# Kernel optimization log

Hardware: AMD Instinct MI355X
Metric: run time of the kernel (lower is better)

Reference implementation:

```python
import jax, jax.numpy as jnp
import numpy as np

N = 100000      # nodes (categories_nums[0])
E = 1600000     # edges
FEAT = 16       # features_num
HID = 32        # hidden
IDE = 16        # id_embed_size
EMB = 8         # embed_size
CAT_MAX = 1000  # categorical vocab (categories_nums[1:])
K = 3           # TAGConv hops (sparse=False)
NC = 2          # num_class
IN_DIM = IDE + 2 * EMB + HID  # 64 -> TAGConv input
EPS = 1e-5


def layer_norm(x, g, b):
    m = jnp.mean(x, axis=-1, keepdims=True)
    v = jnp.mean((x - m) ** 2, axis=-1, keepdims=True)
    return (x - m) * jax.lax.rsqrt(v + EPS) * g + b


def setup_inputs() -> dict:
    key = jax.random.key(0)
    ks = jax.random.split(key, 20)
    s = 0.05
    return {
        "x": jax.random.normal(ks[0], (N, FEAT), jnp.float32),
        "edge_index": jax.random.randint(ks[1], (2, E), 0, N, jnp.int64),
        "edge_weight": jax.random.uniform(ks[2], (E,), jnp.float32),
        "categories_value": jax.random.randint(ks[3], (N, 3), 0, CAT_MAX, jnp.int64),
        "id_table": jax.random.normal(ks[4], (N, IDE), jnp.float32) * s,
        "lin0_id_W": jax.random.normal(ks[5], (IDE, IDE), jnp.float32) * s,
        "lin0_id_b": jnp.zeros((IDE,), jnp.float32),
        "emb1": jax.random.normal(ks[6], (CAT_MAX, EMB), jnp.float32) * s,
        "emb2": jax.random.normal(ks[7], (CAT_MAX, EMB), jnp.float32) * s,
        "lin0_emb_W": jax.random.normal(ks[8], (2 * EMB, 2 * EMB), jnp.float32) * s,
        "lin0_emb_b": jnp.zeros((2 * EMB,), jnp.float32),
        "lin0_W": jax.random.normal(ks[9], (FEAT, HID), jnp.float32) * s,
        "lin0_b": jnp.zeros((HID,), jnp.float32),
        "ln0_g": jnp.ones((IN_DIM,), jnp.float32),
        "ln0_b": jnp.zeros((IN_DIM,), jnp.float32),
        "tag_W": jax.random.normal(ks[10], (K + 1, IN_DIM, HID), jnp.float32) * s,
        "tag_b": jnp.zeros((HID,), jnp.float32),
        "ln1_g": jnp.ones((HID,), jnp.float32),
        "ln1_b": jnp.zeros((HID,), jnp.float32),
        "lin1_W": jax.random.normal(ks[11], (HID, NC), jnp.float32) * s,
        "lin1_b": jnp.zeros((NC,), jnp.float32),
    }


def reference(x, edge_index, edge_weight, categories_value, id_table, lin0_id_W,
              lin0_id_b, emb1, emb2, lin0_emb_W, lin0_emb_b, lin0_W, lin0_b,
              ln0_g, ln0_b, tag_W, tag_b, ln1_g, ln1_b, lin1_W, lin1_b):
    # eval mode: dropouts are identity
    h = jax.nn.elu(x @ lin0_W + lin0_b)                       # [N, HID]
    ide = id_table[categories_value[:, 0]]                    # [N, IDE]
    ide = jax.nn.elu(ide @ lin0_id_W + lin0_id_b)
    er = jnp.concatenate([emb1[categories_value[:, 1]],
                          emb2[categories_value[:, 2]]], axis=1)  # [N, 2*EMB]
    er = jax.nn.elu(er @ lin0_emb_W + lin0_emb_b)
    feat = jnp.concatenate([ide, h, er], axis=1)              # [N, IN_DIM]
    feat = layer_norm(feat, ln0_g, ln0_b)

    # TAGConv: gcn_norm without self-loops, K-hop propagation
    row, col = edge_index[0], edge_index[1]                   # source -> target
    deg = jax.ops.segment_sum(edge_weight, col, num_segments=N)
    dis = jnp.where(deg > 0, deg ** -0.5, 0.0)
    norm = dis[row] * edge_weight * dis[col]                  # [E]

    out = feat @ tag_W[0]                                     # [N, HID]
    xk = feat
    for k in range(1, K + 1):
        xk = jax.ops.segment_sum(xk[row] * norm[:, None], col, num_segments=N)
        out = out + xk @ tag_W[k]
    out = out + tag_b

    out = jax.nn.relu(out)
    out = layer_norm(out, ln1_g, ln1_b)
    out = out @ lin1_W + lin1_b                               # [N, NC]
    return jax.nn.log_softmax(out, axis=-1)
```

## Files before the change

kernel.cpp:

```cpp
#include <hip/hip_runtime.h>
#include <hip/hip_bf16.h>

typedef unsigned short u16;
typedef unsigned int   u32;
typedef unsigned long long u64;
typedef u32 u32x2 __attribute__((ext_vector_type(2)));
typedef u32 u32x4 __attribute__((ext_vector_type(4)));

#define FIX_SCALE 16777216.0f
#define FIX_INV   (1.0f / 16777216.0f)
#define CNT_SHIFT 40
#define DEG_MASK  ((1ULL << CNT_SHIFT) - 1)

__device__ __forceinline__ float b2f(u16 u) { return __uint_as_float(((u32)u) << 16); }
__device__ __forceinline__ u16 f2b(float f) {
    u32 u = __float_as_uint(f);
    return (u16)((u + 0x7FFFu + ((u >> 16) & 1u)) >> 16);
}
__device__ __forceinline__ float elu(float v) { return v > 0.f ? v : expm1f(v); }
__device__ __forceinline__ float ldf(const void* p, size_t i, int f32) {
    return f32 ? ((const float*)p)[i] : b2f(((const u16*)p)[i]);
}
__device__ __forceinline__ float plo(u32 a) { return __uint_as_float(a << 16); }
__device__ __forceinline__ float phi(u32 a) { return __uint_as_float(a & 0xFFFF0000u); }

__global__ void k_flags(const u32* __restrict__ gw, const int* __restrict__ ei,
                        const int* __restrict__ cat, int* __restrict__ flags) {
    if (threadIdx.x == 0 && blockIdx.x == 0) {
        flags[0] = (gw[0] == 0x3F800000u) ? 1 : 0;
        flags[1] = ((ei[1]  | ei[3]  | ei[5]  | ei[7])  == 0) ? 2 : 1;
        flags[2] = ((cat[1] | cat[3] | cat[5] | cat[7]) == 0) ? 2 : 1;
    }
}

__global__ __launch_bounds__(256) void k_feathist(
    const void* __restrict__ x, const int* __restrict__ cat,
    const void* __restrict__ id_table, const void* __restrict__ W_id, const void* __restrict__ b_id,
    const void* __restrict__ emb1, const void* __restrict__ emb2,
    const void* __restrict__ W_emb, const void* __restrict__ b_emb,
    const void* __restrict__ W0, const void* __restrict__ b0,
    const void* __restrict__ g0, const void* __restrict__ bb0,
    u32* __restrict__ feat,
    const int* __restrict__ ei, const void* __restrict__ ew,
    u64* __restrict__ packed, u16* __restrict__ rank,
    const int* __restrict__ flags, int N, int E, int nbN)
{
    __shared__ float sW0[512];
    __shared__ float sb0[32];
    __shared__ float sWid[256];
    __shared__ float sbid[16];
    __shared__ float sWe[256];
    __shared__ float sbe[16];
    __shared__ float sg[64], sb[64];
    int tid = threadIdx.x;
    int f32 = flags[0], s = flags[1], cs = flags[2];

    int e0 = blockIdx.x * 512 + tid;
    int e1 = e0 + 256;
    u64 old0 = 0, old1 = 0;
    bool h0 = (e0 < E), h1 = (e1 < E);
    const int* colp = ei + (size_t)E * s;
    if (h0) {
        int cdst = colp[(size_t)e0 * s];
        float w = ldf(ew, e0, f32);
        old0 = atomicAdd(&packed[cdst], (1ULL << CNT_SHIFT) | (u64)(w * FIX_SCALE + 0.5f));
    }
    if (h1) {
        int cdst = colp[(size_t)e1 * s];
        float w = ldf(ew, e1, f32);
        old1 = atomicAdd(&packed[cdst], (1ULL << CNT_SHIFT) | (u64)(w * FIX_SCALE + 0.5f));
    }

    if (blockIdx.x < nbN) {
        for (int i = tid; i < 512; i += 256) sW0[i] = ldf(W0, i, f32);
        if (tid < 32) sb0[tid] = ldf(b0, tid, f32);
        sWid[tid] = ldf(W_id, tid, f32);
        if (tid < 16) sbid[tid] = ldf(b_id, tid, f32);
        sWe[tid] = ldf(W_emb, tid, f32);
        if (tid < 16) sbe[tid] = ldf(b_emb, tid, f32);
        if (tid < 64) { sg[tid] = ldf(g0, tid, f32); sb[tid] = ldf(bb0, tid, f32); }
        __syncthreads();

        int i = blockIdx.x * 256 + tid;
        if (i < N) {
            size_t cb = (size_t)i * 3 * cs;
            int c0 = cat[cb], c1 = cat[cb + cs], c2 = cat[cb + 2 * cs];
            float f[64];
            {
                float t[16];
                #pragma unroll
                for (int q = 0; q < 16; q++) t[q] = ldf(id_table, (size_t)c0 * 16 + q, f32);
                #pragma unroll
                for (int j = 0; j < 16; j++) {
                    float a = sbid[j];
                    #pragma unroll
                    for (int ff = 0; ff < 16; ff++) a += t[ff] * sWid[ff * 16 + j];
                    f[j] = elu(a);
                }
            }
            {
                float t[16];
                #pragma unroll
                for (int q = 0; q < 16; q++) t[q] = ldf(x, (size_t)i * 16 + q, f32);
                #pragma unroll
                for (int j = 0; j < 32; j++) {
                    float a = sb0[j];
                    #pragma unroll
                    for (int ff = 0; ff < 16; ff++) a += t[ff] * sW0[ff * 32 + j];
                    f[16 + j] = elu(a);
                }
            }
            {
                float t[16];
                #pragma unroll
                for (int q = 0; q < 8; q++) t[q] = ldf(emb1, (size_t)c1 * 8 + q, f32);
                #pragma unroll
                for (int q = 0; q < 8; q++) t[8 + q] = ldf(emb2, (size_t)c2 * 8 + q, f32);
                #pragma unroll
                for (int j = 0; j < 16; j++) {
                    float a = sbe[j];
                    #pragma unroll
                    for (int ff = 0; ff < 16; ff++) a += t[ff] * sWe[ff * 16 + j];
                    f[48 + j] = elu(a);
                }
            }
            float m = 0.f;
            #pragma unroll
            for (int d = 0; d < 64; d++) m += f[d];
            m *= (1.f / 64.f);
            float var = 0.f;
            #pragma unroll
            for (int d = 0; d < 64; d++) { float df = f[d] - m; var += df * df; }
            var *= (1.f / 64.f);
            float rs = rsqrtf(var + 1e-5f);
            #pragma unroll
            for (int d = 0; d < 64; d++) f[d] = (f[d] - m) * rs * sg[d] + sb[d];

            u32* fp = feat + (size_t)i * 32;
            #pragma unroll
            for (int q = 0; q < 32; q++) fp[q] = ((u32)f2b(f[2 * q + 1]) << 16) | f2b(f[2 * q]);
        }
    }
    if (h0) rank[e0] = (u16)(old0 >> CNT_SHIFT);
    if (h1) rank[e1] = (u16)(old1 >> CNT_SHIFT);
}

__global__ __launch_bounds__(256) void k_zproj(
    const u32* __restrict__ feat, const void* __restrict__ tagW,
    float* __restrict__ oacc, u32* __restrict__ z1, u32* __restrict__ z2, u32* __restrict__ z3,
    const int* __restrict__ flags, int N)
{
    __shared__ float sT[4 * 2056];
    __shared__ u32x4 sF[256];
    __shared__ float sO[1024];
    __shared__ u32   sZ[3 * 512];
    int tid = threadIdx.x;
    int f32 = flags[0];
    for (int i = tid; i < 8192; i += 256) {
        int k = i >> 11, r = i & 2047;
        sT[k * 2056 + r] = ldf(tagW, i, f32);
    }
    int fbase = blockIdx.x * 256;
    sF[tid] = (fbase + tid < N * 8) ? ((const u32x4*)feat)[fbase + tid] : (u32x4){0, 0, 0, 0};
    __syncthreads();

    int nl = tid >> 3;
    int sub = tid & 7, kk = sub >> 1, h = sub & 1;

    float o[16];
    #pragma unroll
    for (int j = 0; j < 16; j++) o[j] = 0.f;
    const float* T = sT + kk * 2056 + h * 16;
    #pragma unroll
    for (int q = 0; q < 8; q++) {
        u32x4 a = sF[nl * 8 + q];
        float f0 = plo(a.x), f1 = phi(a.x);
        float f2 = plo(a.y), f3 = phi(a.y);
        float f4 = plo(a.z), f5 = phi(a.z);
        float f6 = plo(a.w), f7 = phi(a.w);
        const float* T0 = T + (8 * q + 0) * 32;
        const float* T1 = T + (8 * q + 1) * 32;
        const float* T2 = T + (8 * q + 2) * 32;
        const float* T3 = T + (8 * q + 3) * 32;
        const float* T4 = T + (8 * q + 4) * 32;
        const float* T5 = T + (8 * q + 5) * 32;
        const float* T6 = T + (8 * q + 6) * 32;
        const float* T7 = T + (8 * q + 7) * 32;
        #pragma unroll
        for (int j = 0; j < 16; j++) {
            o[j] += f0 * T0[j] + f1 * T1[j] + f2 * T2[j] + f3 * T3[j]
                  + f4 * T4[j] + f5 * T5[j] + f6 * T6[j] + f7 * T7[j];
        }
    }

    if (kk == 0) {
        #pragma unroll
        for (int j = 0; j < 16; j++) sO[nl * 32 + h * 16 + j] = o[j];
    } else {
        u32* zs = sZ + (kk - 1) * 512 + nl * 16 + h * 8;
        #pragma unroll
        for (int jj = 0; jj < 8; jj++) zs[jj] = ((u32)f2b(o[2 * jj + 1]) << 16) | f2b(o[2 * jj]);
    }
    __syncthreads();

    int nv = N - blockIdx.x * 32; if (nv > 32) nv = 32;
    if ((tid >> 3) < nv) {
        ((float4*)oacc)[(size_t)blockIdx.x * 256 + tid] = ((const float4*)sO)[tid];
        ((u32x2*)z1)[(size_t)blockIdx.x * 256 + tid] = ((const u32x2*)sZ)[tid];
        ((u32x2*)z2)[(size_t)blockIdx.x * 256 + tid] = ((const u32x2*)sZ)[256 + tid];
        ((u32x2*)z3)[(size_t)blockIdx.x * 256 + tid] = ((const u32x2*)sZ)[512 + tid];
    }
}

__global__ __launch_bounds__(256) void k_scan1(const u64* __restrict__ packed, int* __restrict__ ebuf,
                                               int* __restrict__ bsum, float* __restrict__ dis, int N)
{
    __shared__ int sdat[256];
    int tid = threadIdx.x;
    int i = blockIdx.x * 256 + tid;
    u64 pv = (i < N) ? packed[i] : 0ULL;
    int v = (int)(pv >> CNT_SHIFT);
    sdat[tid] = v;
    __syncthreads();
    for (int off = 1; off < 256; off <<= 1) {
        int t = (tid >= off) ? sdat[tid - off] : 0;
        __syncthreads();
        sdat[tid] += t;
        __syncthreads();
    }
    if (i < N) {
        ebuf[i] = sdat[tid] - v;
        u64 db = pv & DEG_MASK;
        dis[i] = db ? rsqrtf((float)db * FIX_INV) : 0.f;
    }
    if (tid == 255) bsum[blockIdx.x] = sdat[255];
}

__global__ __launch_bounds__(512) void k_scan2(const int* __restrict__ bsum, int* __restrict__ boff, int NB)
{
    __shared__ int sdat[512];
    __shared__ int scarry;
    int tid = threadIdx.x;
    if (tid == 0) scarry = 0;
    __syncthreads();
    for (int base = 0; base < NB; base += 512) {
        int i = base + tid;
        int v = (i < NB) ? bsum[i] : 0;
        sdat[tid] = v;
        __syncthreads();
        for (int off = 1; off < 512; off <<= 1) {
            int t = (tid >= off) ? sdat[tid - off] : 0;
            __syncthreads();
            sdat[tid] += t;
            __syncthreads();
        }
        if (i < NB) boff[i] = scarry + sdat[tid] - v;
        __syncthreads();
        if (tid == 0) scarry += sdat[511];
        __syncthreads();
    }
}

__global__ __launch_bounds__(256) void k_scan3(const int* __restrict__ ebuf, const int* __restrict__ boff,
                                               int* __restrict__ rowptr, int N, int E)
{
    int i = blockIdx.x * 256 + threadIdx.x;
    if (i >= N) return;
    rowptr[i] = boff[blockIdx.x] + ebuf[i];
    if (i == N - 1) rowptr[N] = E;
}

__global__ __launch_bounds__(256) void k_scatter(const int* __restrict__ ei, const void* __restrict__ ew,
                                                 const float* __restrict__ dis, const u16* __restrict__ rank,
                                                 const int* __restrict__ rowptr, int2* __restrict__ csr,
                                                 const int* __restrict__ flags, int E)
{
    int f32 = flags[0], s = flags[1];
    const int* row = ei;
    const int* col = ei + (size_t)E * s;
    int e = blockIdx.x * 256 + threadIdx.x;
    if (e >= E) return;
    int r = row[(size_t)e * s], c = col[(size_t)e * s];
    float nrm = dis[r] * ldf(ew, e, f32) * dis[c];
    csr[rowptr[c] + (int)rank[e]] = make_int2(r, __float_as_int(nrm));
}

template<int ADD>
__global__ __launch_bounds__(256) void k_ahop(
    const u32* __restrict__ zin, const u32* __restrict__ zadd, u32* __restrict__ uout,
    const int* __restrict__ rowptr, const int2* __restrict__ csr, int N)
{
    int tid = threadIdx.x;
    int node = blockIdx.x * 4 + (tid >> 6);
    if (node >= N) return;
    int lane = tid & 63;
    int o = (lane >> 3) & 7;
    int c = lane & 7;
    int start = rowptr[node], end = rowptr[node + 1];

    const u32x2* fin2 = (const u32x2*)zin;
    float v0 = 0.f, v1 = 0.f, v2 = 0.f, v3 = 0.f;
    int e = start;
    for (; e + 16 <= end; e += 16) {
        int2 ma = csr[e + o];
        int2 mb = csr[e + 8 + o];
        u32x2 aa = fin2[(size_t)(u32)ma.x * 8 + c];
        u32x2 ab = fin2[(size_t)(u32)mb.x * 8 + c];
        float wa = __int_as_float(ma.y), wb = __int_as_float(mb.y);
        v0 += plo(aa.x) * wa; v1 += phi(aa.x) * wa; v2 += plo(aa.y) * wa; v3 += phi(aa.y) * wa;
        v0 += plo(ab.x) * wb; v1 += phi(ab.x) * wb; v2 += plo(ab.y) * wb; v3 += phi(ab.y) * wb;
    }
    for (; e < end; e += 8) {
        int ee = e + o;
        int2 m = (ee < end) ? csr[ee] : make_int2(0, 0);
        u32x2 a = fin2[(size_t)(u32)m.x * 8 + c];
        float w = __int_as_float(m.y);
        v0 += plo(a.x) * w; v1 += phi(a.x) * w; v2 += plo(a.y) * w; v3 += phi(a.y) * w;
    }
    v0 += __shfl_xor(v0, 8);  v1 += __shfl_xor(v1, 8);  v2 += __shfl_xor(v2, 8);  v3 += __shfl_xor(v3, 8);
    v0 += __shfl_xor(v0, 16); v1 += __shfl_xor(v1, 16); v2 += __shfl_xor(v2, 16); v3 += __shfl_xor(v3, 16);
    v0 += __shfl_xor(v0, 32); v1 += __shfl_xor(v1, 32); v2 += __shfl_xor(v2, 32); v3 += __shfl_xor(v3, 32);

    if (lane < 8) {
        if (ADD) {
            u32x2 z = ((const u32x2*)zadd)[(size_t)node * 8 + lane];
            v0 += plo(z.x); v1 += phi(z.x); v2 += plo(z.y); v3 += phi(z.y);
        }
        u32x2 pw;
        pw.x = ((u32)f2b(v1) << 16) | f2b(v0);
        pw.y = ((u32)f2b(v3) << 16) | f2b(v2);
        ((u32x2*)uout)[(size_t)node * 8 + lane] = pw;
    }
}

__global__ __launch_bounds__(256) void k_head(
    const float* __restrict__ oacc, const u32* __restrict__ t1,
    const void* __restrict__ tag_b,
    const void* __restrict__ g1, const void* __restrict__ b1,
    const void* __restrict__ W1, const void* __restrict__ bb1,
    void* __restrict__ out, const int* __restrict__ flags, int N)
{
    __shared__ float stb[32], sg[32], sbb[32], sW1[64], sb1v[2];
    int tid = threadIdx.x;
    int f32 = flags[0];
    if (tid < 32) { stb[tid] = ldf(tag_b, tid, f32); sg[tid] = ldf(g1, tid, f32); sbb[tid] = ldf(b1, tid, f32); }
    if (tid < 64) sW1[tid] = ldf(W1, tid, f32);
    if (tid < 2) sb1v[tid] = ldf(bb1, tid, f32);
    __syncthreads();

    int i = blockIdx.x * 256 + tid;
    if (i >= N) return;

    float acc[32];
    const float4* oa4 = (const float4*)(oacc + (size_t)i * 32);
    #pragma unroll
    for (int q = 0; q < 8; q++) {
        float4 t = oa4[q];
        acc[4 * q] = t.x; acc[4 * q + 1] = t.y; acc[4 * q + 2] = t.z; acc[4 * q + 3] = t.w;
    }
    const u32x2* tp = (const u32x2*)t1 + (size_t)i * 8;
    #pragma unroll
    for (int q = 0; q < 8; q++) {
        u32x2 z = tp[q];
        acc[4 * q]     += plo(z.x); acc[4 * q + 1] += phi(z.x);
        acc[4 * q + 2] += plo(z.y); acc[4 * q + 3] += phi(z.y);
    }
    float o[32]; float m = 0.f;
    #pragma unroll
    for (int j = 0; j < 32; j++) { float t = acc[j] + stb[j]; t = t > 0.f ? t : 0.f; o[j] = t; m += t; }
    m *= (1.f / 32.f);
    float var = 0.f;
    #pragma unroll
    for (int j = 0; j < 32; j++) { float d = o[j] - m; var += d * d; }
    var *= (1.f / 32.f);
    float rs = rsqrtf(var + 1e-5f);
    float z0 = sb1v[0], z1 = sb1v[1];
    #pragma unroll
    for (int j = 0; j < 32; j++) {
        float t = (o[j] - m) * rs * sg[j] + sbb[j];
        z0 += t * sW1[2 * j];
        z1 += t * sW1[2 * j + 1];
    }
    float mx = fmaxf(z0, z1);
    float l = mx + logf(expf(z0 - mx) + expf(z1 - mx));
    if (f32) {
        ((float*)out)[(size_t)i * 2]     = z0 - l;
        ((float*)out)[(size_t)i * 2 + 1] = z1 - l;
    } else {
        *((u32*)((u16*)out + (size_t)i * 2)) = ((u32)f2b(z1 - l) << 16) | f2b(z0 - l);
    }
}

extern "C" void kernel_launch(void* const* d_in, const int* in_sizes, int n_in,
                              void* d_out, int out_size, void* d_ws, size_t ws_size,
                              hipStream_t stream)
{
    const void* x        = d_in[0];
    const int*  ei       = (const int*)d_in[1];
    const void* ew       = d_in[2];
    const int*  cat      = (const int*)d_in[3];
    const void* id_table = d_in[4];
    const void* W_id     = d_in[5];
    const void* b_id     = d_in[6];
    const void* emb1     = d_in[7];
    const void* emb2     = d_in[8];
    const void* W_emb    = d_in[9];
    const void* b_emb    = d_in[10];
    const void* W0       = d_in[11];
    const void* b0       = d_in[12];
    const void* g0       = d_in[13];
    const void* bb0      = d_in[14];
    const void* tagW     = d_in[15];
    const void* tag_b    = d_in[16];
    const void* g1       = d_in[17];
    const void* b1       = d_in[18];
    const void* W1       = d_in[19];
    const void* bb1      = d_in[20];

    int N = in_sizes[0] / 16;
    int E = in_sizes[2];
    int nb = (N + 255) / 256;
    int eb = (E + 255) / 256;
    int eb2 = (E + 511) / 512;
    int zb = (N + 31) / 32;

    char* ws = (char*)d_ws;
    size_t off = 0;
    int*   flags  = (int*)(ws + off);   off += 256;
    float* oacc   = (float*)(ws + off); off += (size_t)N * 32 * 4;
    u32*   feat   = (u32*)(ws + off);   off += (size_t)N * 32 * 4;
    u32*   z1     = (u32*)(ws + off);   off += (size_t)N * 16 * 4;
    u32*   z2     = (u32*)(ws + off);   off += (size_t)N * 16 * 4;
    u32*   z3     = (u32*)(ws + off);   off += (size_t)N * 16 * 4;
    u32*   u2     = (u32*)(ws + off);   off += (size_t)N * 16 * 4;
    int2*  csr    = (int2*)(ws + off);  off += (size_t)E * 8;
    int*   rowptr = (int*)(ws + off);   off += ((size_t)N + 1) * 4;
    off = (off + 255) & ~(size_t)255;
    u16*   rank   = (u16*)(ws + off);   off += (size_t)E * 2;
    off = (off + 255) & ~(size_t)255;
    u64*   packed = (u64*)(ws + off);   off += (size_t)N * 8;
    int*   ebuf   = (int*)(ws + off);   off += (size_t)N * 4;
    float* dis    = (float*)(ws + off); off += (size_t)N * 4;
    int*   bsum   = (int*)(ws + off);   off += (size_t)nb * 4;
    int*   boff   = (int*)(ws + off);   off += (size_t)nb * 4;

    hipMemsetAsync(packed, 0, (size_t)N * 8, stream);
    k_flags<<<1, 64, 0, stream>>>((const u32*)g0, ei, cat, flags);

    k_feathist<<<eb2, 256, 0, stream>>>(x, cat, id_table, W_id, b_id, emb1, emb2, W_emb, b_emb,
                                        W0, b0, g0, bb0, feat,
                                        ei, ew, packed, rank, flags, N, E, nb);
    k_zproj<<<zb, 256, 0, stream>>>(feat, tagW, oacc, z1, z2, z3, flags, N);

    k_scan1<<<nb, 256, 0, stream>>>(packed, ebuf, bsum, dis, N);
    k_scan2<<<1, 512, 0, stream>>>(bsum, boff, nb);
    k_scan3<<<nb, 256, 0, stream>>>(ebuf, boff, rowptr, N, E);
    k_scatter<<<eb, 256, 0, stream>>>(ei, ew, dis, rank, rowptr, csr, flags, E);

    int hb = (N + 3) / 4;
    k_ahop<1><<<hb, 256, 0, stream>>>(z3, z2, u2, rowptr, csr, N);
    k_ahop<1><<<hb, 256, 0, stream>>>(u2, z1, z3, rowptr, csr, N);
    k_ahop<0><<<hb, 256, 0, stream>>>(z3, z1, z2, rowptr, csr, N);
    k_head<<<nb, 256, 0, stream>>>(oacc, z2, tag_b, g1, b1, W1, bb1, d_out, flags, N);
}
```

Baseline: 417.9 us.

## Split hop feature arrays into column halves to shrink gather working set

Result: slower. 558.8 us (+33.7%).

```diff
diff --git a/kernel.cpp b/kernel.cpp
--- a/kernel.cpp
+++ b/kernel.cpp
@@ -147,7 +147,10 @@
 
 __global__ __launch_bounds__(256) void k_zproj(
     const u32* __restrict__ feat, const void* __restrict__ tagW,
-    float* __restrict__ oacc, u32* __restrict__ z1, u32* __restrict__ z2, u32* __restrict__ z3,
+    float* __restrict__ oacc,
+    u32* __restrict__ z1A, u32* __restrict__ z1B,
+    u32* __restrict__ z2A, u32* __restrict__ z2B,
+    u32* __restrict__ z3A, u32* __restrict__ z3B,
     const int* __restrict__ flags, int N)
 {
     __shared__ float sT[4 * 2056];
@@ -197,7 +200,7 @@
         #pragma unroll
         for (int j = 0; j < 16; j++) sO[nl * 32 + h * 16 + j] = o[j];
     } else {
-        u32* zs = sZ + (kk - 1) * 512 + nl * 16 + h * 8;
+        u32* zs = sZ + (kk - 1) * 512 + h * 256 + nl * 8;
         #pragma unroll
         for (int jj = 0; jj < 8; jj++) zs[jj] = ((u32)f2b(o[2 * jj + 1]) << 16) | f2b(o[2 * jj]);
     }
@@ -206,9 +209,17 @@
     int nv = N - blockIdx.x * 32; if (nv > 32) nv = 32;
     if ((tid >> 3) < nv) {
         ((float4*)oacc)[(size_t)blockIdx.x * 256 + tid] = ((const float4*)sO)[tid];
-        ((u32x2*)z1)[(size_t)blockIdx.x * 256 + tid] = ((const u32x2*)sZ)[tid];
-        ((u32x2*)z2)[(size_t)blockIdx.x * 256 + tid] = ((const u32x2*)sZ)[256 + tid];
-        ((u32x2*)z3)[(size_t)blockIdx.x * 256 + tid] = ((const u32x2*)sZ)[512 + tid];
+    }
+    {
+        int half = tid >> 7;
+        int idx  = tid & 127;
+        int nl2  = idx >> 2;
+        if (nl2 < nv) {
+            size_t gi = (size_t)blockIdx.x * 128 + idx;
+            ((u32x2*)(half ? z1B : z1A))[gi] = ((const u32x2*)(sZ + 0 * 512 + half * 256))[idx];
+            ((u32x2*)(half ? z2B : z2A))[gi] = ((const u32x2*)(sZ + 1 * 512 + half * 256))[idx];
+            ((u32x2*)(half ? z3B : z3A))[gi] = ((const u32x2*)(sZ + 2 * 512 + half * 256))[idx];
+        }
     }
 }
 
@@ -282,7 +293,9 @@
     if (e >= E) return;
     int r = row[(size_t)e * s], c = col[(size_t)e * s];
     float nrm = dis[r] * ldf(ew, e, f32) * dis[c];
-    csr[rowptr[c] + (int)rank[e]] = make_int2(r, __float_as_int(nrm));
+    int rk = (int)__builtin_nontemporal_load(rank + e);
+    u64 val = ((u64)(u32)__float_as_int(nrm) << 32) | (u32)r;
+    __builtin_nontemporal_store(val, (u64*)csr + (size_t)(rowptr[c] + rk));
 }
 
 template<int ADD>
@@ -290,51 +303,66 @@
     const u32* __restrict__ zin, const u32* __restrict__ zadd, u32* __restrict__ uout,
     const int* __restrict__ rowptr, const int2* __restrict__ csr, int N)
 {
+    __shared__ u32x2 sOut[16];
     int tid = threadIdx.x;
-    int node = blockIdx.x * 4 + (tid >> 6);
-    if (node >= N) return;
+    int wid = tid >> 6;
+    int node = blockIdx.x * 4 + wid;
     int lane = tid & 63;
-    int o = (lane >> 3) & 7;
-    int c = lane & 7;
-    int start = rowptr[node], end = rowptr[node + 1];
+    int g = lane >> 2;
+    int c = lane & 3;
+    bool live = (node < N);
+    int nodec = live ? node : (N - 1);
+    int start = __builtin_nontemporal_load(rowptr + nodec);
+    int end   = __builtin_nontemporal_load(rowptr + nodec + 1);
 
     const u32x2* fin2 = (const u32x2*)zin;
+    const u64* csr64 = (const u64*)csr;
     float v0 = 0.f, v1 = 0.f, v2 = 0.f, v3 = 0.f;
     int e = start;
-    for (; e + 16 <= end; e += 16) {
-        int2 ma = csr[e + o];
-        int2 mb = csr[e + 8 + o];
-        u32x2 aa = fin2[(size_t)(u32)ma.x * 8 + c];
-        u32x2 ab = fin2[(size_t)(u32)mb.x * 8 + c];
-        float wa = __int_as_float(ma.y), wb = __int_as_float(mb.y);
+    for (; e + 32 <= end; e += 32) {
+        u64 ma = __builtin_nontemporal_load(csr64 + e + g);
+        u64 mb = __builtin_nontemporal_load(csr64 + e + 16 + g);
+        u32x2 aa = fin2[(size_t)(u32)(ma & 0xFFFFFFFFu) * 4 + c];
+        u32x2 ab = fin2[(size_t)(u32)(mb & 0xFFFFFFFFu) * 4 + c];
+        float wa = __uint_as_float((u32)(ma >> 32));
+        float wb = __uint_as_float((u32)(mb >> 32));
         v0 += plo(aa.x) * wa; v1 += phi(aa.x) * wa; v2 += plo(aa.y) * wa; v3 += phi(aa.y) * wa;
         v0 += plo(ab.x) * wb; v1 += phi(ab.x) * wb; v2 += plo(ab.y) * wb; v3 += phi(ab.y) * wb;
     }
-    for (; e < end; e += 8) {
-        int ee = e + o;
-        int2 m = (ee < end) ? csr[ee] : make_int2(0, 0);
-        u32x2 a = fin2[(size_t)(u32)m.x * 8 + c];
-        float w = __int_as_float(m.y);
+    for (; e < end; e += 16) {
+        int ee = e + g;
+        u64 m = (ee < end) ? __builtin_nontemporal_load(csr64 + ee) : 0ULL;
+        u32x2 a = fin2[(size_t)(u32)(m & 0xFFFFFFFFu) * 4 + c];
+        float w = __uint_as_float((u32)(m >> 32));
         v0 += plo(a.x) * w; v1 += phi(a.x) * w; v2 += plo(a.y) * w; v3 += phi(a.y) * w;
     }
+    v0 += __shfl_xor(v0, 4);  v1 += __shfl_xor(v1, 4);  v2 += __shfl_xor(v2, 4);  v3 += __shfl_xor(v3, 4);
     v0 += __shfl_xor(v0, 8);  v1 += __shfl_xor(v1, 8);  v2 += __shfl_xor(v2, 8);  v3 += __shfl_xor(v3, 8);
     v0 += __shfl_xor(v0, 16); v1 += __shfl_xor(v1, 16); v2 += __shfl_xor(v2, 16); v3 += __shfl_xor(v3, 16);
     v0 += __shfl_xor(v0, 32); v1 += __shfl_xor(v1, 32); v2 += __shfl_xor(v2, 32); v3 += __shfl_xor(v3, 32);
 
-    if (lane < 8) {
+    if (lane < 4) {
         if (ADD) {
-            u32x2 z = ((const u32x2*)zadd)[(size_t)node * 8 + lane];
-            v0 += plo(z.x); v1 += phi(z.x); v2 += plo(z.y); v3 += phi(z.y);
+            u64 zz = __builtin_nontemporal_load((const u64*)zadd + (size_t)nodec * 4 + c);
+            u32 zlo = (u32)zz, zhi = (u32)(zz >> 32);
+            v0 += plo(zlo); v1 += phi(zlo); v2 += plo(zhi); v3 += phi(zhi);
         }
         u32x2 pw;
         pw.x = ((u32)f2b(v1) << 16) | f2b(v0);
         pw.y = ((u32)f2b(v3) << 16) | f2b(v2);
-        ((u32x2*)uout)[(size_t)node * 8 + lane] = pw;
+        sOut[wid * 4 + c] = pw;
+    }
+    __syncthreads();
+    if (tid < 16) {
+        int nodew = blockIdx.x * 4 + (tid >> 2);
+        if (nodew < N) {
+            __builtin_nontemporal_store(sOut[tid], (u32x2*)uout + (size_t)blockIdx.x * 16 + tid);
+        }
     }
 }
 
 __global__ __launch_bounds__(256) void k_head(
-    const float* __restrict__ oacc, const u32* __restrict__ t1,
+    const float* __restrict__ oacc, const u32* __restrict__ t1A, const u32* __restrict__ t1B,
     const void* __restrict__ tag_b,
     const void* __restrict__ g1, const void* __restrict__ b1,
     const void* __restrict__ W1, const void* __restrict__ bb1,
@@ -358,12 +386,19 @@
         float4 t = oa4[q];
         acc[4 * q] = t.x; acc[4 * q + 1] = t.y; acc[4 * q + 2] = t.z; acc[4 * q + 3] = t.w;
     }
-    const u32x2* tp = (const u32x2*)t1 + (size_t)i * 8;
-    #pragma unroll
-    for (int q = 0; q < 8; q++) {
-        u32x2 z = tp[q];
+    const u32x2* tA = (const u32x2*)t1A + (size_t)i * 4;
+    const u32x2* tB = (const u32x2*)t1B + (size_t)i * 4;
+    #pragma unroll
+    for (int q = 0; q < 4; q++) {
+        u32x2 z = tA[q];
         acc[4 * q]     += plo(z.x); acc[4 * q + 1] += phi(z.x);
         acc[4 * q + 2] += plo(z.y); acc[4 * q + 3] += phi(z.y);
+    }
+    #pragma unroll
+    for (int q = 0; q < 4; q++) {
+        u32x2 z = tB[q];
+        acc[16 + 4 * q]     += plo(z.x); acc[16 + 4 * q + 1] += phi(z.x);
+        acc[16 + 4 * q + 2] += plo(z.y); acc[16 + 4 * q + 3] += phi(z.y);
     }
     float o[32]; float m = 0.f;
     #pragma unroll
@@ -429,10 +464,14 @@
     int*   flags  = (int*)(ws + off);   off += 256;
     float* oacc   = (float*)(ws + off); off += (size_t)N * 32 * 4;
     u32*   feat   = (u32*)(ws + off);   off += (size_t)N * 32 * 4;
-    u32*   z1     = (u32*)(ws + off);   off += (size_t)N * 16 * 4;
-    u32*   z2     = (u32*)(ws + off);   off += (size_t)N * 16 * 4;
-    u32*   z3     = (u32*)(ws + off);   off += (size_t)N * 16 * 4;
-    u32*   u2     = (u32*)(ws + off);   off += (size_t)N * 16 * 4;
+    u32*   z1A    = (u32*)(ws + off);   off += (size_t)N * 8 * 4;
+    u32*   z1B    = (u32*)(ws + off);   off += (size_t)N * 8 * 4;
+    u32*   z2A    = (u32*)(ws + off);   off += (size_t)N * 8 * 4;
+    u32*   z2B    = (u32*)(ws + off);   off += (size_t)N * 8 * 4;
+    u32*   z3A    = (u32*)(ws + off);   off += (size_t)N * 8 * 4;
+    u32*   z3B    = (u32*)(ws + off);   off += (size_t)N * 8 * 4;
+    u32*   uA     = (u32*)(ws + off);   off += (size_t)N * 8 * 4;
+    u32*   uB     = (u32*)(ws + off);   off += (size_t)N * 8 * 4;
     int2*  csr    = (int2*)(ws + off);  off += (size_t)E * 8;
     int*   rowptr = (int*)(ws + off);   off += ((size_t)N + 1) * 4;
     off = (off + 255) & ~(size_t)255;
@@ -450,7 +489,7 @@
     k_feathist<<<eb2, 256, 0, stream>>>(x, cat, id_table, W_id, b_id, emb1, emb2, W_emb, b_emb,
                                         W0, b0, g0, bb0, feat,
                                         ei, ew, packed, rank, flags, N, E, nb);
-    k_zproj<<<zb, 256, 0, stream>>>(feat, tagW, oacc, z1, z2, z3, flags, N);
+    k_zproj<<<zb, 256, 0, stream>>>(feat, tagW, oacc, z1A, z1B, z2A, z2B, z3A, z3B, flags, N);
 
     k_scan1<<<nb, 256, 0, stream>>>(packed, ebuf, bsum, dis, N);
     k_scan2<<<1, 512, 0, stream>>>(bsum, boff, nb);
@@ -458,8 +497,11 @@
     k_scatter<<<eb, 256, 0, stream>>>(ei, ew, dis, rank, rowptr, csr, flags, E);
 
     int hb = (N + 3) / 4;
-    k_ahop<1><<<hb, 256, 0, stream>>>(z3, z2, u2, rowptr, csr, N);
-    k_ahop<1><<<hb, 256, 0, stream>>>(u2, z1, z3, rowptr, csr, N);
-    k_ahop<0><<<hb, 256, 0, stream>>>(z3, z1, z2, rowptr, csr, N);
-    k_head<<<nb, 256, 0, stream>>>(oacc, z2, tag_b, g1, b1, W1, bb1, d_out, flags, N);
-}
+    k_ahop<1><<<hb, 256, 0, stream>>>(z3A, z2A, uA, rowptr, csr, N);
+    k_ahop<1><<<hb, 256, 0, stream>>>(z3B, z2B, uB, rowptr, csr, N);
+    k_ahop<1><<<hb, 256, 0, stream>>>(uA, z1A, z3A, rowptr, csr, N);
+    k_ahop<1><<<hb, 256, 0, stream>>>(uB, z1B, z3B, rowptr, csr, N);
+    k_ahop<0><<<hb, 256, 0, stream>>>(z3A, z1A, z2A, rowptr, csr, N);
+    k_ahop<0><<<hb, 256, 0, stream>>>(z3B, z1B, z2B, rowptr, csr, N);
+    k_head<<<nb, 256, 0, stream>>>(oacc, z2A, z2B, tag_b, g1, b1, W1, bb1, d_out, flags, N);
+}
```
